# Optimization experiments

Measured on AMD Instinct MI355X. Metric: run time of the kernel, lower is better.

The kernel has to match this reference:

```python
import jax, jax.numpy as jnp
import numpy as np

N_E = 1024
E_DIM = 256
BETA = 0.25
DECAY = 0.99
EPS = 1e-5


def setup_inputs() -> dict:
    key = jax.random.key(0)
    k1, k2 = jax.random.split(key)
    z = jax.random.normal(k1, (16, E_DIM, 64, 64), dtype=jnp.float32)
    # embedding.weight.data.uniform_(-1/n_e, 1/n_e)
    weight = jax.random.uniform(k2, (N_E, E_DIM), dtype=jnp.float32,
                                minval=-1.0 / N_E, maxval=1.0 / N_E)
    cluster_size = jnp.zeros((N_E,), dtype=jnp.float32)
    embedding_avg = weight  # clone of initial weight
    return {"z": z, "weight": weight, "cluster_size": cluster_size,
            "embedding_avg": embedding_avg}


def reference(z, weight, cluster_size, embedding_avg):
    B, C, H, W = z.shape  # C == e_dim
    zp = jnp.transpose(z, (0, 2, 3, 1))          # [B,H,W,C]
    zf = zp.reshape(-1, C)                       # [N, C], N = B*H*W

    # ||z||^2 + ||e||^2 - 2 z e^T  -> [N, n_e]
    d = (jnp.sum(zf * zf, axis=1, keepdims=True)
         + jnp.sum(weight * weight, axis=1)
         - 2.0 * jnp.matmul(zf, weight.T))
    idx = jnp.argmin(d, axis=1)                  # [N] int

    z_q = weight[idx].reshape(zp.shape)          # [B,H,W,C]

    # EMA codebook update (training branch), computed with scatter-sums
    n_e = weight.shape[0]
    counts = jax.ops.segment_sum(jnp.ones(zf.shape[0], dtype=zf.dtype),
                                 idx, num_segments=n_e)        # encodings.sum(0)
    new_cluster_size = cluster_size * DECAY + (1.0 - DECAY) * counts
    n = jnp.sum(new_cluster_size)
    cs_smoothed = (new_cluster_size + EPS) / (n + n_e * EPS) * n
    dw = jax.ops.segment_sum(zf, idx, num_segments=n_e)        # encodings.T @ zf
    new_embedding_avg = embedding_avg * DECAY + (1.0 - DECAY) * dw
    new_weight = new_embedding_avg / cs_smoothed[:, None]

    loss = BETA * jnp.mean((jax.lax.stop_gradient(z_q) - zp) ** 2)
    z_q_st = zp + jax.lax.stop_gradient(z_q - zp)   # straight-through
    out = jnp.transpose(z_q_st, (0, 3, 1, 2))        # back to NCHW
    return out, loss, idx, new_cluster_size, new_embedding_avg, new_weight
```

## Files before the change

### kernel.cpp

```cpp
#include <hip/hip_runtime.h>
#include <hip/hip_bf16.h>

typedef unsigned short ushort_t;
typedef __attribute__((ext_vector_type(8))) _Float16 half8;
typedef __attribute__((ext_vector_type(4))) _Float16 half4;
typedef __attribute__((ext_vector_type(4))) float f32x4;

#define NB    16
#define NC    256
#define NHW   4096
#define NPIX  65536
#define NE    1024
#define BETA  0.25f
#define DECAY 0.99f
#define EPS_  1e-5f
#define GAP_FLAG 1.25e-4f

#define OFF_LOSS 16777216
#define OFF_IDXF 16777217
#define OFF_NCS  16842753
#define OFF_NEA  16843777
#define OFF_NW   17105921

#define WS_WSUM  0
#define WS_CSSM  1024
#define WS_LPART 2048
#define WS_CNT   4096
#define WS_FLAGS 4128
#define WS_LIST  6176
#define WS_WF16  40960
#define WS_ZF16  (WS_WF16 + 131072)
#define WS_IDXI  (WS_ZF16 + 8388608)
#define WS_CCNT  (WS_IDXI + 65536)
#define WS_OFFS  (WS_CCNT + 1024)
#define WS_CUR   (WS_OFFS + 1024)
#define WS_SORT  (WS_CUR + 1024)
#define WS_END   (WS_SORT + 65536)

__device__ __forceinline__ float sq_nofma(float x) {
    float s = x * x;
    asm volatile("" : "+v"(s));
    return s;
}

__device__ __forceinline__ float np_pair128_sq(const float* __restrict__ a) {
    float r[8];
    #pragma unroll
    for (int m = 0; m < 8; ++m) r[m] = sq_nofma(a[m]);
    for (int i = 8; i < 128; i += 8) {
        #pragma unroll
        for (int m = 0; m < 8; ++m) r[m] += sq_nofma(a[i + m]);
    }
    return ((r[0] + r[1]) + (r[2] + r[3])) + ((r[4] + r[5]) + (r[6] + r[7]));
}

__device__ __forceinline__ void gload16(const void* g, void* ldsp) {
    __builtin_amdgcn_global_load_lds((const __attribute__((address_space(1))) unsigned int*)g,
                                     (__attribute__((address_space(3))) unsigned int*)ldsp,
                                     16, 0, 0);
}

__global__ __launch_bounds__(64) void wsum_kernel(const float* __restrict__ w,
                                                  float* __restrict__ wsum,
                                                  float* __restrict__ ncs,
                                                  int* __restrict__ cnt,
                                                  int* __restrict__ ccount,
                                                  float* __restrict__ lpart) {
    int j = blockIdx.x * 64 + threadIdx.x;
    const float* wr = w + (size_t)j * NC;
    wsum[j] = np_pair128_sq(wr) + np_pair128_sq(wr + 128);
    ncs[j] = 0.0f;
    ccount[j] = 0;
    lpart[j] = 0.0f;
    lpart[j + 1024] = 0.0f;
    if (j == 0) cnt[0] = 0;
}

__global__ __launch_bounds__(256) void wpack_kernel(const float* __restrict__ w,
                                                    _Float16* __restrict__ wf) {
    int i = blockIdx.x * 256 + threadIdx.x;
    wf[i] = (_Float16)(w[i] * 1024.0f);
}

__global__ __launch_bounds__(256) void zpack_kernel(const float* __restrict__ z,
                                                    _Float16* __restrict__ zf) {
    __shared__ float zs[64 * 65];
    const int t = threadIdx.x;
    const int P0 = blockIdx.x * 64;
    const int b = P0 >> 12, hw0 = P0 & (NHW - 1);
    const int K0 = blockIdx.y * 64;
    const int hw = t & 63, cq = t >> 6;
    const float* zb = z + (size_t)b * (NC * NHW) + hw0 + hw;
    #pragma unroll
    for (int i = 0; i < 16; ++i) {
        int kl = cq * 16 + i;
        zs[hw * 65 + kl] = zb[(size_t)(K0 + kl) * NHW];
    }
    __syncthreads();
    const int p = t >> 2, kq = t & 3;
    size_t obase = (size_t)(P0 + p) * NC + K0 + kq * 16;
    #pragma unroll
    for (int h2 = 0; h2 < 2; ++h2) {
        half8 v;
        #pragma unroll
        for (int j2 = 0; j2 < 8; ++j2)
            v[j2] = (_Float16)zs[p * 65 + kq * 16 + h2 * 8 + j2];
        *(half8*)&zf[obase + h2 * 8] = v;
    }
}

__global__ __launch_bounds__(256) void gemm2_kernel(const _Float16* __restrict__ wf,
                                                    const _Float16* __restrict__ zf,
                                                    const float* __restrict__ wsum,
                                                    float* __restrict__ idxf,
                                                    int* __restrict__ idxi,
                                                    ushort_t* __restrict__ list,
                                                    int* __restrict__ cnt,
                                                    float* __restrict__ ncs,
                                                    int* __restrict__ ccount) {
    __shared__ __align__(16) _Float16 zt[128 * 256];
    __shared__ __align__(16) _Float16 wt[128 * 32];
    __shared__ float bvx[256], svx[256];
    __shared__ int   bix[256];
    __shared__ float rbv[128], rsv[128];
    __shared__ int   rbi[128];

    const int t = threadIdx.x;
    const int l = t & 63;
    const int w = t >> 6;
    const int P0 = blockIdx.x * 128;
    const int wc = w >> 1, wp = w & 1;

    #pragma unroll
    for (int i = 0; i < 16; ++i) {
        int row = w * 32 + i * 2 + (l >> 5);
        int gc = (l & 31) ^ (row & 7);
        gload16(zf + (size_t)(P0 + row) * NC + gc * 8,
                &zt[w * 8192 + i * 512 + l * 8]);
    }
    if (t < 128) { rbv[t] = 3.4e38f; rsv[t] = 3.4e38f; rbi[t] = 0; }
    __syncthreads();

    for (int ct = 0; ct < 8; ++ct) {
        f32x4 acc[4][4];
        #pragma unroll
        for (int m = 0; m < 4; ++m)
            #pragma unroll
            for (int n = 0; n < 4; ++n)
                #pragma unroll
                for (int e = 0; e < 4; ++e) acc[m][n][e] = 0.0f;

        for (int ks = 0; ks < 8; ++ks) {
            if (ks) __syncthreads();
            #pragma unroll
            for (int i = 0; i < 2; ++i) {
                int row = w * 32 + i * 16 + (l >> 2);
                int gc = (l & 3) ^ ((l >> 3) & 3);
                gload16(wf + (size_t)(ct * 128 + row) * NC + ks * 32 + gc * 8,
                        &wt[w * 1024 + i * 512 + l * 8]);
            }
            __syncthreads();

            half8 a[4], b[4];
            #pragma unroll
            for (int m = 0; m < 4; ++m) {
                int row = wc * 64 + m * 16 + (l & 15);
                int g = (l >> 4) ^ ((row >> 1) & 3);
                a[m] = *(const half8*)&wt[row * 32 + g * 8];
            }
            #pragma unroll
            for (int n = 0; n < 4; ++n) {
                int row = wp * 64 + n * 16 + (l & 15);
                int chunk = (ks * 4 + (l >> 4)) ^ (row & 7);
                b[n] = *(const half8*)&zt[row * 256 + chunk * 8];
            }
            #pragma unroll
            for (int m = 0; m < 4; ++m)
                #pragma unroll
                for (int n = 0; n < 4; ++n)
                    acc[m][n] = __builtin_amdgcn_mfma_f32_16x16x32_f16(a[m], b[n], acc[m][n], 0, 0, 0);
        }

        float en[4][4];
        #pragma unroll
        for (int m = 0; m < 4; ++m)
            #pragma unroll
            for (int r = 0; r < 4; ++r)
                en[m][r] = wsum[ct * 128 + wc * 64 + m * 16 + (l >> 4) * 4 + r];

        #pragma unroll
        for (int n = 0; n < 4; ++n) {
            float bv = 3.4e38f, sv = 3.4e38f;
            int bi = 0;
            #pragma unroll
            for (int m = 0; m < 4; ++m)
                #pragma unroll
                for (int r = 0; r < 4; ++r) {
                    float s = en[m][r] - acc[m][n][r] * 0.001953125f;
                    int code = ct * 128 + wc * 64 + m * 16 + (l >> 4) * 4 + r;
                    if (s < bv) { sv = bv; bv = s; bi = code; }
                    else if (s < sv) sv = s;
                }
            #pragma unroll
            for (int x = 16; x <= 32; x <<= 1) {
                float v2 = __shfl_xor(bv, x);
                float s2 = __shfl_xor(sv, x);
                int   i2 = __shfl_xor(bi, x);
                if (v2 < bv || (v2 == bv && i2 < bi)) { sv = fminf(bv, s2); bv = v2; bi = i2; }
                else sv = fminf(sv, v2);
            }
            if ((l >> 4) == 0) {
                int lp = wp * 64 + n * 16 + l;
                bvx[wc * 128 + lp] = bv;
                svx[wc * 128 + lp] = sv;
                bix[wc * 128 + lp] = bi;
            }
        }
        __syncthreads();
        if (t < 128) {
            float bv = bvx[t], sv = svx[t];
            int bi = bix[t];
            float v2 = bvx[128 + t], s2 = svx[128 + t];
            int i2 = bix[128 + t];
            if (v2 < bv || (v2 == bv && i2 < bi)) { sv = fminf(bv, s2); bv = v2; bi = i2; }
            else sv = fminf(sv, v2);
            if (bv < rbv[t]) { rsv[t] = fminf(rbv[t], sv); rbv[t] = bv; rbi[t] = bi; }
            else rsv[t] = fminf(rsv[t], bv);
        }
        __syncthreads();
    }

    int* h = (int*)zt;
    #pragma unroll
    for (int e = 0; e < 4; ++e) h[t + e * 256] = 0;
    __syncthreads();
    if (t < 128) {
        int pix = P0 + t;
        idxf[pix] = (float)rbi[t];
        idxi[pix] = rbi[t];
        atomicAdd(&h[rbi[t]], 1);
        if (rsv[t] - rbv[t] < GAP_FLAG) {
            int pos = atomicAdd(cnt, 1);
            list[pos] = (ushort_t)pix;
        }
    }
    __syncthreads();
    #pragma unroll
    for (int e = 0; e < 4; ++e) {
        int v = h[t + e * 256];
        if (v) {
            atomicAdd(&ncs[t + e * 256], (float)v);
            atomicAdd(&ccount[t + e * 256], v);
        }
    }
}

__global__ __launch_bounds__(256) void argmin_kernel(const float* __restrict__ z,
                                                     const float* __restrict__ w,
                                                     const float* __restrict__ enorm,
                                                     float* __restrict__ idxf,
                                                     int* __restrict__ idxi,
                                                     unsigned long long* __restrict__ flags) {
    __shared__ __align__(16) float smem[64 * 68 + 128 * 68];
    float* zt = smem;
    float* wt = smem + 64 * 68;
    const int t = threadIdx.x;
    const int pr = t & 7;
    const int cr = t >> 3;
    const int P0 = blockIdx.x * 64;
    const int b = P0 >> 12;
    const int hw0 = P0 & (NHW - 1);
    const float* zb = z + (size_t)b * (NC * NHW) + hw0;
    float bestv[8], secv[8];
    int besti[8];
    #pragma unroll
    for (int i = 0; i < 8; ++i) { bestv[i] = 3.4e38f; secv[i] = 3.4e38f; besti[i] = 0; }
    for (int cc = 0; cc < 8; ++cc) {
        float acc[8][4];
        #pragma unroll
        for (int i = 0; i < 8; ++i)
            #pragma unroll
            for (int j = 0; j < 4; ++j) acc[i][j] = 0.0f;
        for (int kc = 0; kc < 4; ++kc) {
            {
                int p = t & 63;
                int k0 = (t >> 6) * 16;
                int f2 = ((p >> 3) & 3) << 2;
                #pragma unroll
                for (int i = 0; i < 16; ++i) {
                    int k = k0 + i;
                    zt[p * 68 + (k ^ f2)] = zb[(size_t)(kc * 64 + k) * NHW + p];
                }
            }
            {
                #pragma unroll
                for (int i = 0; i < 8; ++i) {
                    int f = t + 256 * i;
                    int jj = f >> 4;
                    int k4 = f & 15;
                    float4 v = *(const float4*)&w[(size_t)(cc * 128 + jj) * NC + kc * 64 + k4 * 4];
                    *(float4*)&wt[jj * 68 + k4 * 4] = v;
                }
            }
            __syncthreads();
            #pragma unroll 2
            for (int k = 0; k < 64; k += 4) {
                float4 za[8], wb[4];
                #pragma unroll
                for (int i = 0; i < 8; ++i)
                    za[i] = *(float4*)&zt[(pr + 8 * i) * 68 + (k ^ ((i & 3) << 2))];
                #pragma unroll
                for (int j = 0; j < 4; ++j)
                    wb[j] = *(float4*)&wt[(cr + 32 * j) * 68 + k];
                #pragma unroll
                for (int i = 0; i < 8; ++i)
                    #pragma unroll
                    for (int j = 0; j < 4; ++j)
                        acc[i][j] += za[i].x * wb[j].x + za[i].y * wb[j].y +
                                     za[i].z * wb[j].z + za[i].w * wb[j].w;
            }
            __syncthreads();
        }
        #pragma unroll
        for (int j = 0; j < 4; ++j) {
            int code = cc * 128 + cr + 32 * j;
            float enj = enorm[code];
            #pragma unroll
            for (int i = 0; i < 8; ++i) {
                float s = enj - 2.0f * acc[i][j];
                if (s < bestv[i]) { secv[i] = bestv[i]; bestv[i] = s; besti[i] = code; }
                else if (s < secv[i]) secv[i] = s;
            }
        }
    }
    float* rv = smem;
    int* ri = (int*)(smem + 2048);
    float* rs = smem + 4096;
    #pragma unroll
    for (int i = 0; i < 8; ++i) {
        int p = pr + 8 * i;
        rv[p * 32 + cr] = bestv[i];
        ri[p * 32 + cr] = besti[i];
        rs[p * 32 + cr] = secv[i];
    }
    __syncthreads();
    if (t < 64) {
        int p = t;
        float bv = rv[p * 32], sv = rs[p * 32];
        int bi = ri[p * 32];
        for (int s2 = 1; s2 < 32; ++s2) {
            float v = rv[p * 32 + s2];
            float v2 = rs[p * 32 + s2];
            int ii = ri[p * 32 + s2];
            if (v < bv) { sv = bv; bv = v; bi = ii; }
            else {
                if (v < sv) sv = v;
                if (v == bv && ii < bi) bi = ii;
            }
            if (v2 < sv) sv = v2;
        }
        idxf[P0 + p] = (float)bi;
        idxi[P0 + p] = bi;
        unsigned long long mask = __ballot((sv - bv) < GAP_FLAG);
        if (t == 0) flags[blockIdx.x] = mask;
    }
}

__global__ __launch_bounds__(256) void gather_kernel(const unsigned long long* __restrict__ flags,
                                                     ushort_t* __restrict__ list,
                                                     int* __restrict__ cnt) {
    int p = blockIdx.x * 256 + threadIdx.x;
    unsigned long long m = flags[p >> 6];
    if ((m >> (p & 63)) & 1ULL) {
        int pos = atomicAdd(cnt, 1);
        list[pos] = (ushort_t)p;
    }
}

__global__ __launch_bounds__(1024) void hist_kernel(const int* __restrict__ idxi,
                                                    float* __restrict__ ncs) {
    __shared__ int h[NE];
    int t = threadIdx.x;
    h[t] = 0;
    __syncthreads();
    int gid = blockIdx.x * 1024 + t;
    #pragma unroll
    for (int i = 0; i < 4; ++i) atomicAdd(&h[idxi[gid + i * 16384]], 1);
    __syncthreads();
    if (h[t]) atomicAdd(&ncs[t], (float)h[t]);
}

__global__ __launch_bounds__(1024, 8) void dwloss_kernel(const float* __restrict__ z,
                                                         const float* __restrict__ w,
                                                         const int* __restrict__ idxi,
                                                         float* __restrict__ dw0,
                                                         float* __restrict__ dw1,
                                                         float* __restrict__ lpart) {
    __shared__ float acc[NE];
    __shared__ float wcol[NE];
    __shared__ float ls[16];
    const int c = blockIdx.x;
    const int part = blockIdx.y;
    const int t = threadIdx.x;
    acc[t] = 0.0f;
    wcol[t] = w[(size_t)t * NC + c];
    __syncthreads();
    const float* zc = z + (size_t)c * NHW;
    float lsum = 0.0f;
    #pragma unroll
    for (int half = 0; half < 2; ++half) {
        float4 zv[4];
        int4   iv[4];
        #pragma unroll
        for (int i = 0; i < 4; ++i) {
            int b = part * 8 + half * 4 + i;
            zv[i] = *(const float4*)&zc[(size_t)b * (NC * NHW) + t * 4];
            iv[i] = *(const int4*)&idxi[b * 4096 + t * 4];
        }
        #pragma unroll
        for (int i = 0; i < 4; ++i) {
            float q0 = wcol[iv[i].x], q1 = wcol[iv[i].y];
            float q2 = wcol[iv[i].z], q3 = wcol[iv[i].w];
            float d0 = q0 - zv[i].x, d1 = q1 - zv[i].y;
            float d2 = q2 - zv[i].z, d3 = q3 - zv[i].w;
            lsum += d0 * d0 + d1 * d1 + d2 * d2 + d3 * d3;
            atomicAdd(&acc[iv[i].x], zv[i].x);
            atomicAdd(&acc[iv[i].y], zv[i].y);
            atomicAdd(&acc[iv[i].z], zv[i].z);
            atomicAdd(&acc[iv[i].w], zv[i].w);
        }
    }
    #pragma unroll
    for (int off = 32; off > 0; off >>= 1) lsum += __shfl_down(lsum, off);
    if ((t & 63) == 0) ls[t >> 6] = lsum;
    __syncthreads();
    if (t == 0) {
        float s = 0.0f;
        #pragma unroll
        for (int q = 0; q < 16; ++q) s += ls[q];
        lpart[c * 2 + part] = s;
    }
    float* dwp = part ? dw1 : dw0;
    dwp[(size_t)t * NC + c] = acc[t];
}

__global__ __launch_bounds__(256) void fixup3_kernel(const float* __restrict__ z,
                                                     const float* __restrict__ w,
                                                     const float* __restrict__ wsum,
                                                     const ushort_t* __restrict__ list,
                                                     const int* __restrict__ cnt,
                                                     float* __restrict__ idxf,
                                                     int* __restrict__ idxi,
                                                     float* __restrict__ ncs,
                                                     int* __restrict__ ccount) {
    const int count = cnt[0];
    if (count == 0) return;
    const int ngroups = (count + 7) >> 3;
    const int t = threadIdx.x;

    __shared__ __align__(16) char smem_raw[16384 + 8192];
    double (*zd)[NC] = (double(*)[NC])smem_raw;
    float  (*zf)[NC] = (float(*)[NC])(smem_raw + 16384);
    float* rbv = (float*)(smem_raw + 16384);
    int*   rbi = (int*)smem_raw;
    __shared__ float zs_sh[8];
    __shared__ int   pix_sh[8];
    __shared__ float r2v[8][32];
    __shared__ int   r2i[8][32];

    for (int g = blockIdx.x; g < ngroups; g += gridDim.x) {
        if (t < 8) {
            int i = g * 8 + t;
            pix_sh[t] = (i < count) ? (int)list[i] : (int)list[0];
        }
        __syncthreads();
        #pragma unroll
        for (int px = 0; px < 8; ++px) {
            int p = pix_sh[px];
            int b = p >> 12, hw = p & (NHW - 1);
            float zv = z[(size_t)b * (NC * NHW) + (size_t)t * NHW + hw];
            zf[px][t] = zv;
            zd[px][t] = (double)zv;
        }
        __syncthreads();
        if (t < 8) zs_sh[t] = np_pair128_sq(zf[t]) + np_pair128_sq(zf[t] + 128);
        __syncthreads();

        float zs_reg[8];
        #pragma unroll
        for (int px = 0; px < 8; ++px) zs_reg[px] = zs_sh[px];

        float bvr[8];
        int   bir[8];
        #pragma unroll
        for (int px = 0; px < 8; ++px) { bvr[px] = 3.4e38f; bir[px] = 0; }

        #pragma unroll
        for (int jo = 0; jo < 2; ++jo) {
            const int j0 = t + jo * 512;
            const int j1 = j0 + 256;
            const float* wr0 = w + (size_t)j0 * NC;
            const float* wr1 = w + (size_t)j1 * NC;
            double acc0[8], acc1[8];
            #pragma unroll
            for (int px = 0; px < 8; ++px) { acc0[px] = 0.0; acc1[px] = 0.0; }
            for (int k = 0; k < NC; k += 4) {
                float4 wa = *(const float4*)&wr0[k];
                float4 wb = *(const float4*)&wr1[k];
                const float* wap = (const float*)&wa;
                const float* wbp = (const float*)&wb;
                #pragma unroll
                for (int e = 0; e < 4; ++e) {
                    double wea = (double)wap[e];
                    double web = (double)wbp[e];
                    #pragma unroll
                    for (int px = 0; px < 8; ++px) {
                        double zv = zd[px][k + e];
                        acc0[px] += wea * zv;
                        acc1[px] += web * zv;
                    }
                }
            }
            float ws0 = wsum[j0], ws1 = wsum[j1];
            #pragma unroll
            for (int px = 0; px < 8; ++px) {
                float m0 = (float)acc0[px];
                float s10 = zs_reg[px] + ws0;
                float d0 = s10 - 2.0f * m0;
                if (d0 < bvr[px] || (d0 == bvr[px] && j0 < bir[px])) { bvr[px] = d0; bir[px] = j0; }
                float m1 = (float)acc1[px];
                float s11 = zs_reg[px] + ws1;
                float d1 = s11 - 2.0f * m1;
                if (d1 < bvr[px] || (d1 == bvr[px] && j1 < bir[px])) { bvr[px] = d1; bir[px] = j1; }
            }
        }
        __syncthreads();
        #pragma unroll
        for (int px = 0; px < 8; ++px) {
            rbv[px * 256 + t] = bvr[px];
            rbi[px * 256 + t] = bir[px];
        }
        __syncthreads();
        {
            int px = t >> 5, s = t & 31;
            float bv = rbv[px * 256 + s * 8];
            int   bi = rbi[px * 256 + s * 8];
            #pragma unroll
            for (int e = 1; e < 8; ++e) {
                float v2 = rbv[px * 256 + s * 8 + e];
                int   i2 = rbi[px * 256 + s * 8 + e];
                if (v2 < bv || (v2 == bv && i2 < bi)) { bv = v2; bi = i2; }
            }
            r2v[px][s] = bv;
            r2i[px][s] = bi;
        }
        __syncthreads();
        if (t < 8) {
            float bv = r2v[t][0];
            int   bi = r2i[t][0];
            for (int s = 1; s < 32; ++s) {
                float v2 = r2v[t][s];
                int   i2 = r2i[t][s];
                if (v2 < bv || (v2 == bv && i2 < bi)) { bv = v2; bi = i2; }
            }
            if (g * 8 + t < count) {
                int p = pix_sh[t];
                int old = idxi[p];
                if (old != bi) {
                    idxf[p] = (float)bi;
                    idxi[p] = bi;
                    atomicAdd(&ncs[old], -1.0f);
                    atomicAdd(&ncs[bi], 1.0f);
                    if (ccount) {
                        atomicAdd(&ccount[old], -1);
                        atomicAdd(&ccount[bi], 1);
                    }
                }
            }
        }
        __syncthreads();
    }
}

__global__ __launch_bounds__(1024, 8) void out2_kernel(const float* __restrict__ w,
                                                       const int* __restrict__ idxi,
                                                       float* __restrict__ outq) {
    __shared__ float wcol[NE];
    const int c = blockIdx.x;
    const int part = blockIdx.y;
    const int t = threadIdx.x;
    wcol[t] = w[(size_t)t * NC + c];
    __syncthreads();
    float* oc = outq + (size_t)c * NHW;
    #pragma unroll
    for (int half = 0; half < 2; ++half) {
        int4 iv[4];
        #pragma unroll
        for (int i = 0; i < 4; ++i) {
            int b = part * 8 + half * 4 + i;
            iv[i] = *(const int4*)&idxi[b * 4096 + t * 4];
        }
        asm volatile("" :: "v"(iv[0].x), "v"(iv[1].x), "v"(iv[2].x), "v"(iv[3].x));
        #pragma unroll
        for (int i = 0; i < 4; ++i) {
            int b = part * 8 + half * 4 + i;
            float4 ov;
            ov.x = wcol[iv[i].x]; ov.y = wcol[iv[i].y];
            ov.z = wcol[iv[i].z]; ov.w = wcol[iv[i].w];
            *(float4*)&oc[(size_t)b * (NC * NHW) + t * 4] = ov;
        }
    }
}

__global__ __launch_bounds__(1024) void scan_kernel(const int* __restrict__ ccount,
                                                    int* __restrict__ offs,
                                                    int* __restrict__ cur) {
    __shared__ int s[1024];
    int t = threadIdx.x;
    int c0 = ccount[t];
    s[t] = c0;
    __syncthreads();
    for (int off = 1; off < 1024; off <<= 1) {
        int v = (t >= off) ? s[t - off] : 0;
        __syncthreads();
        s[t] += v;
        __syncthreads();
    }
    int ex = s[t] - c0;
    offs[t] = ex;
    cur[t] = ex;
}

__global__ __launch_bounds__(256) void scatter2_kernel(const int* __restrict__ idxi,
                                                       int* __restrict__ cur,
                                                       int* __restrict__ sorted) {
    int p = blockIdx.x * 256 + threadIdx.x;
    int id = idxi[p];
    int pos = atomicAdd(&cur[id], 1);
    sorted[pos] = p;
}

__global__ __launch_bounds__(256) void dwsum2_kernel(const _Float16* __restrict__ zf,
                                                     const float* __restrict__ w,
                                                     const int* __restrict__ sorted,
                                                     const int* __restrict__ offs,
                                                     const int* __restrict__ ccount,
                                                     float* __restrict__ dw0,
                                                     float* __restrict__ dw1,
                                                     float* __restrict__ lpart) {
    const int t = threadIdx.x, l = t & 63, wv = t >> 6;
    const int j = blockIdx.x * 4 + wv;
    const int part = blockIdx.y;
    const float4 q = *(const float4*)&w[(size_t)j * NC + l * 4];
    const int start = offs[j], cntj = ccount[j];
    const int h0 = (cntj + 1) >> 1;
    const int s = part ? start + h0 : start;
    const int e = part ? start + cntj : start + h0;
    float a0 = 0.f, a1 = 0.f, a2 = 0.f, a3 = 0.f, lsum = 0.f;
    for (int base = s; base < e; base += 64) {
        int pm = (base + l < e) ? sorted[base + l] : 0;
        int nn = min(64, e - base);
        for (int i = 0; i < nn; ++i) {
            int p = __shfl(pm, i);
            half4 zv = *(const half4*)&zf[(size_t)p * NC + l * 4];
            float z0 = (float)zv[0], z1 = (float)zv[1];
            float z2 = (float)zv[2], z3 = (float)zv[3];
            a0 += z0; a1 += z1; a2 += z2; a3 += z3;
            float d0 = q.x - z0, d1 = q.y - z1, d2 = q.z - z2, d3 = q.w - z3;
            lsum += d0 * d0 + d1 * d1 + d2 * d2 + d3 * d3;
        }
    }
    float* dwp = part ? dw1 : dw0;
    float4 av = make_float4(a0, a1, a2, a3);
    *(float4*)&dwp[(size_t)j * NC + l * 4] = av;
    #pragma unroll
    for (int off = 32; off > 0; off >>= 1) lsum += __shfl_down(lsum, off);
    if (l == 0) lpart[j * 2 + part] = lsum;
}

__global__ __launch_bounds__(1024) void finalize_kernel(const float* __restrict__ cs,
                                                        const float* __restrict__ lpart,
                                                        float* __restrict__ ncs,
                                                        float* __restrict__ cssm,
                                                        float* __restrict__ loss) {
    int t = threadIdx.x;
    float cnt = ncs[t];
    float v = cs[t] * DECAY + (1.0f - DECAY) * cnt;
    ncs[t] = v;
    __shared__ float red[1024];
    red[t] = v;
    __syncthreads();
    for (int s = 512; s > 0; s >>= 1) {
        if (t < s) red[t] += red[t + s];
        __syncthreads();
    }
    float n = red[0];
    __syncthreads();
    cssm[t] = (v + EPS_) / (n + (float)NE * EPS_) * n;
    red[t] = lpart[t] + lpart[t + 1024];
    __syncthreads();
    for (int s = 512; s > 0; s >>= 1) {
        if (t < s) red[t] += red[t + s];
        __syncthreads();
    }
    if (t == 0) loss[0] = BETA * red[0] / 16777216.0f;
}

__global__ __launch_bounds__(256) void neaw_kernel(const float* __restrict__ ea,
                                                   const float* __restrict__ cssm,
                                                   float* __restrict__ nea,
                                                   float* __restrict__ nw) {
    int lin = blockIdx.x * 256 + threadIdx.x;
    float dw = nea[lin] + nw[lin];
    float v = DECAY * ea[lin] + (1.0f - DECAY) * dw;
    nea[lin] = v;
    nw[lin] = v / cssm[lin >> 8];
}

extern "C" void kernel_launch(void* const* d_in, const int* in_sizes, int n_in,
                              void* d_out, int out_size, void* d_ws, size_t ws_size,
                              hipStream_t stream) {
    const float* z  = (const float*)d_in[0];
    const float* w  = (const float*)d_in[1];
    const float* cs = (const float*)d_in[2];
    const float* ea = (const float*)d_in[3];

    float* out  = (float*)d_out;
    float* loss = out + OFF_LOSS;
    float* idxf = out + OFF_IDXF;
    float* ncs  = out + OFF_NCS;
    float* nea  = out + OFF_NEA;
    float* nw   = out + OFF_NW;

    float* wsf = (float*)d_ws;
    float* wsum = wsf + WS_WSUM;
    float* cssm = wsf + WS_CSSM;
    float* lpart = wsf + WS_LPART;
    int* cnt = (int*)(wsf + WS_CNT);
    unsigned long long* flags = (unsigned long long*)(wsf + WS_FLAGS);
    ushort_t* list = (ushort_t*)(wsf + WS_LIST);
    int* idxi = (int*)(wsf + WS_IDXI);
    int* ccount = (int*)(wsf + WS_CCNT);
    int* offs = (int*)(wsf + WS_OFFS);
    int* cur = (int*)(wsf + WS_CUR);
    int* sorted = (int*)(wsf + WS_SORT);

    const bool fast = ws_size >= (size_t)WS_END * 4;

    hipLaunchKernelGGL(wsum_kernel, dim3(16), dim3(64), 0, stream, w, wsum, ncs, cnt,
                       fast ? ccount : cnt, lpart);

    if (fast) {
        _Float16* wf16 = (_Float16*)(wsf + WS_WF16);
        _Float16* zf16 = (_Float16*)(wsf + WS_ZF16);
        hipLaunchKernelGGL(wpack_kernel, dim3(1024), dim3(256), 0, stream, w, wf16);
        hipLaunchKernelGGL(zpack_kernel, dim3(1024, 4), dim3(256), 0, stream, z, zf16);
        hipLaunchKernelGGL(gemm2_kernel, dim3(512), dim3(256), 0, stream,
                           wf16, zf16, wsum, idxf, idxi, list, cnt, ncs, ccount);
        hipLaunchKernelGGL(fixup3_kernel, dim3(256), dim3(256), 0, stream,
                           z, w, wsum, list, cnt, idxf, idxi, ncs, ccount);
        hipLaunchKernelGGL(out2_kernel, dim3(256, 2), dim3(1024), 0, stream, w, idxi, out);
        hipLaunchKernelGGL(scan_kernel, dim3(1), dim3(1024), 0, stream, ccount, offs, cur);
        hipLaunchKernelGGL(scatter2_kernel, dim3(256), dim3(256), 0, stream, idxi, cur, sorted);
        hipLaunchKernelGGL(dwsum2_kernel, dim3(256, 2), dim3(256), 0, stream,
                           zf16, w, sorted, offs, ccount, nea, nw, lpart);
    } else {
        hipLaunchKernelGGL(argmin_kernel, dim3(1024), dim3(256), 0, stream, z, w, wsum, idxf, idxi, flags);
        hipLaunchKernelGGL(gather_kernel, dim3(256), dim3(256), 0, stream, flags, list, cnt);
        hipLaunchKernelGGL(hist_kernel, dim3(16), dim3(1024), 0, stream, idxi, ncs);
        hipLaunchKernelGGL(fixup3_kernel, dim3(256), dim3(256), 0, stream,
                           z, w, wsum, list, cnt, idxf, idxi, ncs, (int*)nullptr);
        hipLaunchKernelGGL(out2_kernel, dim3(256, 2), dim3(1024), 0, stream, w, idxi, out);
        hipLaunchKernelGGL(dwloss_kernel, dim3(256, 2), dim3(1024), 0, stream, z, w, idxi, nea, nw, lpart);
    }

    hipLaunchKernelGGL(finalize_kernel, dim3(1), dim3(1024), 0, stream, cs, lpart, ncs, cssm, loss);
    hipLaunchKernelGGL(neaw_kernel, dim3(1024), dim3(256), 0, stream, ea, cssm, nea, nw);
}
```

Baseline: 263.4 us.

## Double-buffer codebook tiles and keep running argmin in registers across tiles

```diff
diff --git a/kernel.cpp b/kernel.cpp
--- a/kernel.cpp
+++ b/kernel.cpp
@@ -118,12 +118,13 @@
                                                     int* __restrict__ cnt,
                                                     float* __restrict__ ncs,
                                                     int* __restrict__ ccount) {
-    __shared__ __align__(16) _Float16 zt[128 * 256];
-    __shared__ __align__(16) _Float16 wt[128 * 32];
-    __shared__ float bvx[256], svx[256];
-    __shared__ int   bix[256];
-    __shared__ float rbv[128], rsv[128];
-    __shared__ int   rbi[128];
+    __shared__ __align__(16) char smem[81920];
+    _Float16* zt = (_Float16*)smem;
+    _Float16* wt = (_Float16*)(smem + 65536);
+    float* bvx = (float*)(smem + 65536);
+    float* svx = bvx + 256;
+    int*   bix = (int*)(svx + 256);
+    int*   h   = (int*)smem;
 
     const int t = threadIdx.x;
     const int l = t & 63;
@@ -131,6 +132,16 @@
     const int P0 = blockIdx.x * 128;
     const int wc = w >> 1, wp = w & 1;
 
+    auto stage_w = [&](int ct, int ks, int buf) {
+        #pragma unroll
+        for (int i = 0; i < 2; ++i) {
+            int row = w * 32 + i * 16 + (l >> 2);
+            int gc = (l & 3) ^ ((l >> 3) & 3);
+            gload16(wf + (size_t)(ct * 128 + row) * NC + ks * 32 + gc * 8,
+                    &wt[buf * 4096 + w * 1024 + i * 512 + l * 8]);
+        }
+    };
+
     #pragma unroll
     for (int i = 0; i < 16; ++i) {
         int row = w * 32 + i * 2 + (l >> 5);
@@ -138,9 +149,16 @@
         gload16(zf + (size_t)(P0 + row) * NC + gc * 8,
                 &zt[w * 8192 + i * 512 + l * 8]);
     }
-    if (t < 128) { rbv[t] = 3.4e38f; rsv[t] = 3.4e38f; rbi[t] = 0; }
-    __syncthreads();
-
+    stage_w(0, 0, 0);
+
+    float rbv2[4], rsv2[4];
+    int   rbi2[4];
+    #pragma unroll
+    for (int n = 0; n < 4; ++n) { rbv2[n] = 3.4e38f; rsv2[n] = 3.4e38f; rbi2[n] = 0; }
+
+    __syncthreads();
+
+    int buf = 0;
     for (int ct = 0; ct < 8; ++ct) {
         f32x4 acc[4][4];
         #pragma unroll
@@ -151,22 +169,17 @@
                 for (int e = 0; e < 4; ++e) acc[m][n][e] = 0.0f;
 
         for (int ks = 0; ks < 8; ++ks) {
-            if (ks) __syncthreads();
-            #pragma unroll
-            for (int i = 0; i < 2; ++i) {
-                int row = w * 32 + i * 16 + (l >> 2);
-                int gc = (l & 3) ^ ((l >> 3) & 3);
-                gload16(wf + (size_t)(ct * 128 + row) * NC + ks * 32 + gc * 8,
-                        &wt[w * 1024 + i * 512 + l * 8]);
-            }
-            __syncthreads();
-
+            int step = ct * 8 + ks;
+            if (step < 63) {
+                int ns = step + 1;
+                stage_w(ns >> 3, ns & 7, buf ^ 1);
+            }
             half8 a[4], b[4];
             #pragma unroll
             for (int m = 0; m < 4; ++m) {
                 int row = wc * 64 + m * 16 + (l & 15);
                 int g = (l >> 4) ^ ((row >> 1) & 3);
-                a[m] = *(const half8*)&wt[row * 32 + g * 8];
+                a[m] = *(const half8*)&wt[buf * 4096 + row * 32 + g * 8];
             }
             #pragma unroll
             for (int n = 0; n < 4; ++n) {
@@ -179,67 +192,60 @@
                 #pragma unroll
                 for (int n = 0; n < 4; ++n)
                     acc[m][n] = __builtin_amdgcn_mfma_f32_16x16x32_f16(a[m], b[n], acc[m][n], 0, 0, 0);
-        }
-
-        float en[4][4];
-        #pragma unroll
-        for (int m = 0; m < 4; ++m)
-            #pragma unroll
-            for (int r = 0; r < 4; ++r)
-                en[m][r] = wsum[ct * 128 + wc * 64 + m * 16 + (l >> 4) * 4 + r];
-
-        #pragma unroll
-        for (int n = 0; n < 4; ++n) {
-            float bv = 3.4e38f, sv = 3.4e38f;
-            int bi = 0;
-            #pragma unroll
-            for (int m = 0; m < 4; ++m)
+            __syncthreads();
+            buf ^= 1;
+        }
+
+        #pragma unroll
+        for (int m = 0; m < 4; ++m) {
+            float4 env = *(const float4*)&wsum[ct * 128 + wc * 64 + m * 16 + (l >> 4) * 4];
+            const float* en = &env.x;
+            #pragma unroll
+            for (int n = 0; n < 4; ++n)
                 #pragma unroll
                 for (int r = 0; r < 4; ++r) {
-                    float s = en[m][r] - acc[m][n][r] * 0.001953125f;
+                    float s = en[r] - acc[m][n][r] * 0.001953125f;
                     int code = ct * 128 + wc * 64 + m * 16 + (l >> 4) * 4 + r;
-                    if (s < bv) { sv = bv; bv = s; bi = code; }
-                    else if (s < sv) sv = s;
+                    if (s < rbv2[n]) { rsv2[n] = rbv2[n]; rbv2[n] = s; rbi2[n] = code; }
+                    else if (s < rsv2[n]) rsv2[n] = s;
                 }
-            #pragma unroll
-            for (int x = 16; x <= 32; x <<= 1) {
-                float v2 = __shfl_xor(bv, x);
-                float s2 = __shfl_xor(sv, x);
-                int   i2 = __shfl_xor(bi, x);
-                if (v2 < bv || (v2 == bv && i2 < bi)) { sv = fminf(bv, s2); bv = v2; bi = i2; }
-                else sv = fminf(sv, v2);
-            }
-            if ((l >> 4) == 0) {
-                int lp = wp * 64 + n * 16 + l;
-                bvx[wc * 128 + lp] = bv;
-                svx[wc * 128 + lp] = sv;
-                bix[wc * 128 + lp] = bi;
-            }
-        }
-        __syncthreads();
-        if (t < 128) {
-            float bv = bvx[t], sv = svx[t];
-            int bi = bix[t];
-            float v2 = bvx[128 + t], s2 = svx[128 + t];
-            int i2 = bix[128 + t];
+        }
+    }
+
+    #pragma unroll
+    for (int n = 0; n < 4; ++n) {
+        float bv = rbv2[n], sv = rsv2[n];
+        int bi = rbi2[n];
+        #pragma unroll
+        for (int x = 16; x <= 32; x <<= 1) {
+            float v2 = __shfl_xor(bv, x);
+            float s2 = __shfl_xor(sv, x);
+            int   i2 = __shfl_xor(bi, x);
             if (v2 < bv || (v2 == bv && i2 < bi)) { sv = fminf(bv, s2); bv = v2; bi = i2; }
             else sv = fminf(sv, v2);
-            if (bv < rbv[t]) { rsv[t] = fminf(rbv[t], sv); rbv[t] = bv; rbi[t] = bi; }
-            else rsv[t] = fminf(rsv[t], bv);
-        }
-        __syncthreads();
-    }
-
-    int* h = (int*)zt;
+        }
+        if ((l >> 4) == 0) {
+            int lp = wp * 64 + n * 16 + l;
+            bvx[wc * 128 + lp] = bv;
+            svx[wc * 128 + lp] = sv;
+            bix[wc * 128 + lp] = bi;
+        }
+    }
     #pragma unroll
     for (int e = 0; e < 4; ++e) h[t + e * 256] = 0;
     __syncthreads();
     if (t < 128) {
+        float bv = bvx[t], sv = svx[t];
+        int bi = bix[t];
+        float v2 = bvx[128 + t], s2 = svx[128 + t];
+        int i2 = bix[128 + t];
+        if (v2 < bv || (v2 == bv && i2 < bi)) { sv = fminf(bv, s2); bv = v2; bi = i2; }
+        else sv = fminf(sv, v2);
         int pix = P0 + t;
-        idxf[pix] = (float)rbi[t];
-        idxi[pix] = rbi[t];
-        atomicAdd(&h[rbi[t]], 1);
-        if (rsv[t] - rbv[t] < GAP_FLAG) {
+        idxf[pix] = (float)bi;
+        idxi[pix] = bi;
+        atomicAdd(&h[bi], 1);
+        if (sv - bv < GAP_FLAG) {
             int pos = atomicAdd(cnt, 1);
             list[pos] = (ushort_t)pix;
         }
```

After: 256.1 us. 1.03x faster.
